# Optimization experiments

Hardware: AMD Instinct MI355X
Metric: run time of the kernel (lower is better)

Reference implementation:

```python
import jax, jax.numpy as jnp
import numpy as np

N = 512
N_B = 32
N_C = 16
NUM_CH = 20


def setup_inputs() -> dict:
    key = jax.random.key(0)
    ks = jax.random.split(key, 9)
    x = jax.random.normal(ks[0], (N, NUM_CH), dtype=jnp.float32)
    # fc1: 20 -> 128
    W1 = jax.random.normal(ks[1], (NUM_CH, 128), dtype=jnp.float32) * (1.0 / np.sqrt(NUM_CH))
    b1 = jnp.zeros((128,), dtype=jnp.float32)
    # fc2: 128 -> 20
    W2 = jax.random.normal(ks[2], (128, NUM_CH), dtype=jnp.float32) * (1.0 / np.sqrt(128))
    b2 = jnp.zeros((NUM_CH,), dtype=jnp.float32)
    # minibatch-discrimination tensor T: (20, n_B*n_C)
    T = jax.random.normal(ks[3], (NUM_CH, N_B * N_C), dtype=jnp.float32) * 0.1
    # fc3: (20 + n_B) -> 1
    W3 = jax.random.normal(ks[4], (NUM_CH + N_B, 1), dtype=jnp.float32) * (1.0 / np.sqrt(NUM_CH + N_B))
    b3 = jnp.zeros((1,), dtype=jnp.float32)
    return {"x": x, "W1": W1, "b1": b1, "W2": W2, "b2": b2, "T": T, "W3": W3, "b3": b3}


def reference(x, W1, b1, W2, b2, T, W3, b3):
    h = jax.nn.relu(x @ W1 + b1)            # (N, 128)
    h = jax.nn.relu(h @ W2 + b2)            # (N, 20)
    M = (h @ T).reshape(-1, N_B, N_C)       # (N, n_B, n_C)
    # pairwise L1 distance over n_C: (N, n_B, n_C, 1) - (1, n_B, n_C, N)
    d = jnp.sum(jnp.abs(M[:, :, :, None] - jnp.transpose(M, (1, 2, 0))[None]), axis=2)  # (N, n_B, N)
    o = jnp.sum(jnp.exp(-d), axis=2)        # (N, n_B)
    o = o - jnp.mean(o)
    feat = jnp.concatenate([h, o], axis=1)  # (N, 20 + n_B)
    return jax.nn.sigmoid(feat @ W3 + b3)   # (N, 1)
```

## Files before the change

kernel.cpp:

```cpp
#include <hip/hip_runtime.h>
#include <math.h>

#define N 512
#define NB 32
#define NC 16
#define CH 20
#define JP 4

#define WS_H 0
#define WS_M 10240
#define WS_OPART 272384

__global__ __launch_bounds__(128) void k1_fwd(
        const float* __restrict__ x,
        const float* __restrict__ W1, const float* __restrict__ b1,
        const float* __restrict__ W2, const float* __restrict__ b2,
        const float* __restrict__ T,
        float* __restrict__ h_g, float* __restrict__ M_g)
{
    const int i = blockIdx.x;
    const int t = threadIdx.x;
    __shared__ float xs[CH];
    __shared__ float h1s[128];
    __shared__ float hs[CH];

    if (t < CH) xs[t] = x[i * CH + t];
    __syncthreads();

    float a = b1[t];
    #pragma unroll
    for (int k = 0; k < CH; ++k) a += xs[k] * W1[k * 128 + t];
    h1s[t] = fmaxf(a, 0.f);
    __syncthreads();

    if (t < CH) {
        float a2 = b2[t];
        #pragma unroll 16
        for (int k = 0; k < 128; ++k) a2 += h1s[k] * W2[k * CH + t];
        a2 = fmaxf(a2, 0.f);
        hs[t] = a2;
        h_g[i * CH + t] = a2;
    }
    __syncthreads();

    #pragma unroll
    for (int r = 0; r < 4; ++r) {
        const int m = t + r * 128;
        float a3 = 0.f;
        #pragma unroll
        for (int k = 0; k < CH; ++k) a3 += hs[k] * T[k * N + m];
        M_g[i * N + m] = a3;
    }
}

__global__ __launch_bounds__(256) void k2_odist(
        const float* __restrict__ M_g, float* __restrict__ opart)
{
    const int t = threadIdx.x;
    const int bidx = blockIdx.x;
    const int b  = bidx & 31;
    const int ic = (bidx >> 5) & 7;
    const int jp = bidx >> 8;

    __shared__ __align__(16) float sj[128][NC];
    __shared__ float red[4][64];

    {
        const int row = t >> 1, half = t & 1;
        const float4* src = reinterpret_cast<const float4*>(
            M_g + (size_t)(jp * 128 + row) * N + b * NC + half * 8);
        float4 v0 = src[0], v1 = src[1];
        float4* dst = reinterpret_cast<float4*>(&sj[row][half * 8]);
        dst[0] = v0; dst[1] = v1;
    }

    const int lane = t & 63;
    const int w = t >> 6;
    const int i = ic * 64 + lane;
    float mi[NC];
    {
        const float4* src = reinterpret_cast<const float4*>(M_g + (size_t)i * N + b * NC);
        float4 a0 = src[0], a1 = src[1], a2 = src[2], a3 = src[3];
        mi[0]=a0.x; mi[1]=a0.y; mi[2]=a0.z; mi[3]=a0.w;
        mi[4]=a1.x; mi[5]=a1.y; mi[6]=a1.z; mi[7]=a1.w;
        mi[8]=a2.x; mi[9]=a2.y; mi[10]=a2.z; mi[11]=a2.w;
        mi[12]=a3.x; mi[13]=a3.y; mi[14]=a3.z; mi[15]=a3.w;
    }
    __syncthreads();

    float acc = 0.f;
    #pragma unroll 4
    for (int jl = 0; jl < 32; ++jl) {
        const float* s = sj[w * 32 + jl];
        float d0 = 0.f, d1 = 0.f, d2 = 0.f, d3 = 0.f;
        #pragma unroll
        for (int c = 0; c < NC; c += 4) {
            d0 += fabsf(mi[c + 0] - s[c + 0]);
            d1 += fabsf(mi[c + 1] - s[c + 1]);
            d2 += fabsf(mi[c + 2] - s[c + 2]);
            d3 += fabsf(mi[c + 3] - s[c + 3]);
        }
        acc += __expf(-((d0 + d1) + (d2 + d3)));
    }

    red[w][lane] = acc;
    __syncthreads();
    if (t < 64) {
        const float s4 = red[0][t] + red[1][t] + red[2][t] + red[3][t];
        opart[((size_t)jp * N + ic * 64 + t) * NB + b] = s4;
    }
}

__global__ __launch_bounds__(512) void k3_final(
        const float* __restrict__ h_g, const float* __restrict__ opart,
        const float* __restrict__ W3, const float* __restrict__ b3,
        float* __restrict__ out)
{
    const int i = threadIdx.x;
    const int lane = i & 63, w = i >> 6;
    __shared__ float sred[8];
    __shared__ float smean;

    float o[NB];
    float oi = 0.f;
    #pragma unroll
    for (int b = 0; b < NB; ++b) {
        float v = opart[(size_t)i * NB + b]
                + opart[(size_t)(N + i) * NB + b]
                + opart[(size_t)(2 * N + i) * NB + b]
                + opart[(size_t)(3 * N + i) * NB + b];
        o[b] = v;
        oi += v;
    }

    float v = oi;
    #pragma unroll
    for (int off = 32; off > 0; off >>= 1) v += __shfl_down(v, off, 64);
    if (lane == 0) sred[w] = v;
    __syncthreads();
    if (i == 0) {
        float tot = 0.f;
        #pragma unroll
        for (int k = 0; k < 8; ++k) tot += sred[k];
        smean = tot * (1.f / (float)(N * NB));
    }
    __syncthreads();
    const float mean = smean;

    float a = b3[0];
    #pragma unroll
    for (int k = 0; k < CH; ++k) a += h_g[i * CH + k] * W3[k];
    #pragma unroll
    for (int b = 0; b < NB; ++b) a += (o[b] - mean) * W3[CH + b];
    out[i] = 1.f / (1.f + __expf(-a));
}

extern "C" void kernel_launch(void* const* d_in, const int* in_sizes, int n_in,
                              void* d_out, int out_size, void* d_ws, size_t ws_size,
                              hipStream_t stream) {
    const float* x  = (const float*)d_in[0];
    const float* W1 = (const float*)d_in[1];
    const float* b1 = (const float*)d_in[2];
    const float* W2 = (const float*)d_in[3];
    const float* b2 = (const float*)d_in[4];
    const float* T  = (const float*)d_in[5];
    const float* W3 = (const float*)d_in[6];
    const float* b3 = (const float*)d_in[7];
    float* out = (float*)d_out;

    float* ws    = (float*)d_ws;
    float* h_g   = ws + WS_H;
    float* M_g   = ws + WS_M;
    float* opart = ws + WS_OPART;

    k1_fwd<<<N, 128, 0, stream>>>(x, W1, b1, W2, b2, T, h_g, M_g);
    k2_odist<<<32 * 8 * JP, 256, 0, stream>>>(M_g, opart);
    k3_final<<<1, 512, 0, stream>>>(h_g, opart, W3, b3, out);
}
```

Baseline: 95.89 us.

## Fold W3 projection into odist kernel via atomics and per-unit sums

The distance kernel now multiplies each partial o value by its W3 weight and atomically accumulates it into a per-row scalar. It also writes one block-level sum per unit for the global mean. The final kernel no longer reads the large partial-o array. It applies the mean algebraically as mean times the sum of the W3 weights, and runs as two blocks. This is meant to cut the final kernel's memory traffic and serial work, at the cost of float atomics and nondeterministic summation order.

```diff
diff --git a/kernel.cpp b/kernel.cpp
--- a/kernel.cpp
+++ b/kernel.cpp
@@ -6,17 +6,20 @@
 #define NC 16
 #define CH 20
 #define JP 4
+#define NUNITS (32 * 8 * JP)
 
 #define WS_H 0
 #define WS_M 10240
-#define WS_OPART 272384
+#define WS_S 272384
+#define WS_USUM 272896
 
 __global__ __launch_bounds__(128) void k1_fwd(
         const float* __restrict__ x,
         const float* __restrict__ W1, const float* __restrict__ b1,
         const float* __restrict__ W2, const float* __restrict__ b2,
         const float* __restrict__ T,
-        float* __restrict__ h_g, float* __restrict__ M_g)
+        float* __restrict__ h_g, float* __restrict__ M_g,
+        float* __restrict__ s_g)
 {
     const int i = blockIdx.x;
     const int t = threadIdx.x;
@@ -24,6 +27,7 @@
     __shared__ float h1s[128];
     __shared__ float hs[CH];
 
+    if (t == 0) s_g[i] = 0.f;
     if (t < CH) xs[t] = x[i * CH + t];
     __syncthreads();
 
@@ -54,13 +58,14 @@
 }
 
 __global__ __launch_bounds__(256) void k2_odist(
-        const float* __restrict__ M_g, float* __restrict__ opart)
+        const float* __restrict__ M_g, const float* __restrict__ W3,
+        float* __restrict__ s_g, float* __restrict__ usum)
 {
     const int t = threadIdx.x;
-    const int bidx = blockIdx.x;
-    const int b  = bidx & 31;
-    const int ic = (bidx >> 5) & 7;
-    const int jp = bidx >> 8;
+    const int unit = blockIdx.x;
+    const int b  = unit & 31;
+    const int ic = (unit >> 5) & 7;
+    const int jp = unit >> 8;
 
     __shared__ __align__(16) float sj[128][NC];
     __shared__ float red[4][64];
@@ -107,51 +112,42 @@
     __syncthreads();
     if (t < 64) {
         const float s4 = red[0][t] + red[1][t] + red[2][t] + red[3][t];
-        opart[((size_t)jp * N + ic * 64 + t) * NB + b] = s4;
+        atomicAdd(&s_g[ic * 64 + t], s4 * W3[CH + b]);
+        float v = s4;
+        #pragma unroll
+        for (int off = 32; off > 0; off >>= 1) v += __shfl_down(v, off, 64);
+        if (t == 0) usum[unit] = v;
     }
 }
 
-__global__ __launch_bounds__(512) void k3_final(
-        const float* __restrict__ h_g, const float* __restrict__ opart,
+__global__ __launch_bounds__(256) void k3_final(
+        const float* __restrict__ h_g, const float* __restrict__ s_g,
+        const float* __restrict__ usum,
         const float* __restrict__ W3, const float* __restrict__ b3,
         float* __restrict__ out)
 {
-    const int i = threadIdx.x;
-    const int lane = i & 63, w = i >> 6;
-    __shared__ float sred[8];
+    const int t = threadIdx.x;
+    const int i = blockIdx.x * 256 + t;
+    const int lane = t & 63, w = t >> 6;
+    __shared__ float sred[4];
     __shared__ float smean;
 
-    float o[NB];
-    float oi = 0.f;
-    #pragma unroll
-    for (int b = 0; b < NB; ++b) {
-        float v = opart[(size_t)i * NB + b]
-                + opart[(size_t)(N + i) * NB + b]
-                + opart[(size_t)(2 * N + i) * NB + b]
-                + opart[(size_t)(3 * N + i) * NB + b];
-        o[b] = v;
-        oi += v;
-    }
-
-    float v = oi;
+    float v = usum[t] + usum[t + 256] + usum[t + 512] + usum[t + 768];
     #pragma unroll
     for (int off = 32; off > 0; off >>= 1) v += __shfl_down(v, off, 64);
     if (lane == 0) sred[w] = v;
     __syncthreads();
-    if (i == 0) {
-        float tot = 0.f;
-        #pragma unroll
-        for (int k = 0; k < 8; ++k) tot += sred[k];
-        smean = tot * (1.f / (float)(N * NB));
-    }
+    if (t == 0) smean = (sred[0] + sred[1] + sred[2] + sred[3]) * (1.f / (float)(N * NB));
     __syncthreads();
     const float mean = smean;
 
-    float a = b3[0];
+    float w3sum = 0.f;
+    #pragma unroll
+    for (int b = 0; b < NB; ++b) w3sum += W3[CH + b];
+
+    float a = b3[0] + s_g[i] - mean * w3sum;
     #pragma unroll
     for (int k = 0; k < CH; ++k) a += h_g[i * CH + k] * W3[k];
-    #pragma unroll
-    for (int b = 0; b < NB; ++b) a += (o[b] - mean) * W3[CH + b];
     out[i] = 1.f / (1.f + __expf(-a));
 }
 
@@ -168,12 +164,13 @@
     const float* b3 = (const float*)d_in[7];
     float* out = (float*)d_out;
 
-    float* ws    = (float*)d_ws;
-    float* h_g   = ws + WS_H;
-    float* M_g   = ws + WS_M;
-    float* opart = ws + WS_OPART;
+    float* ws   = (float*)d_ws;
+    float* h_g  = ws + WS_H;
+    float* M_g  = ws + WS_M;
+    float* s_g  = ws + WS_S;
+    float* usum = ws + WS_USUM;
 
-    k1_fwd<<<N, 128, 0, stream>>>(x, W1, b1, W2, b2, T, h_g, M_g);
-    k2_odist<<<32 * 8 * JP, 256, 0, stream>>>(M_g, opart);
-    k3_final<<<1, 512, 0, stream>>>(h_g, opart, W3, b3, out);
+    k1_fwd<<<N, 128, 0, stream>>>(x, W1, b1, W2, b2, T, h_g, M_g, s_g);
+    k2_odist<<<NUNITS, 256, 0, stream>>>(M_g, W3, s_g, usum);
+    k3_final<<<2, 256, 0, stream>>>(h_g, s_g, usum, W3, b3, out);
 }
```

After: 86.78 us. 1.1x faster.
